# Kernel tuning notes

Hardware: AMD Instinct MI355X
Metric: run time of the kernel (lower is better)

## Reference

```python
import jax, jax.numpy as jnp
import numpy as np

C = 19
IGNORE = 255
UPPER_BOUND = 1.0
SEG_W, EDGE_W, ATT_W = 1.0, 0.3, 0.1
EDGE_THRESH = 0.8


def _img_hist(t):
    # torch.histc(target, bins=C, min=0, max=C): bin i counts values in [i, i+1); 255 falls outside
    tf = t.ravel()
    inb = (tf >= 0) & (tf < C)
    idx = jnp.where(inb, tf, 0)
    return jnp.zeros((C,), jnp.float32).at[idx].add(inb.astype(jnp.float32))


def _seg_loss(segin, target):
    # per-image class-histogram weights (ImageBasedCrossEntropyLoss2d, norm=False)
    N = target.shape[0]
    bins = jax.vmap(_img_hist)(target)                      # [N, C]
    hist_norm = bins / jnp.sum(bins, axis=1, keepdims=True)
    w = (bins != 0).astype(jnp.float32) * UPPER_BOUND * (1.0 - hist_norm) + 1.0  # [N, C]

    logp = jax.nn.log_softmax(segin, axis=1)                # [N, C, H, W]
    tc = jnp.clip(target, 0, C - 1)
    lp = jnp.take_along_axis(logp, tc[:, None, :, :], axis=1)[:, 0]  # [N, H, W]
    valid = (target != IGNORE).astype(jnp.float32)
    pw = jnp.take_along_axis(w, tc.reshape(N, -1), axis=1).reshape(target.shape) * valid
    # NLLLoss(weight, reduction='mean', ignore_index): weighted mean per image, summed over batch
    num = -jnp.sum(pw * lp, axis=(1, 2))
    den = jnp.sum(pw, axis=(1, 2))
    return jnp.sum(num / den)


def _bce2d(x, t):
    # x: logits [N,1,H,W]; t: float target, 1=pos, 0=neg, >1 ignored (weight 0)
    pos = t == 1.0
    neg = t == 0.0
    pos_num = jnp.sum(pos.astype(jnp.float32))
    neg_num = jnp.sum(neg.astype(jnp.float32))
    sum_num = pos_num + neg_num
    w = jnp.where(pos, neg_num / sum_num, 0.0) + jnp.where(neg, pos_num / sum_num, 0.0)
    # stable BCE-with-logits
    bce = jnp.maximum(x, 0.0) - x * t + jnp.log1p(jnp.exp(-jnp.abs(x)))
    return jnp.mean(w * bce)


def setup_inputs() -> dict:
    key = jax.random.key(0)
    k1, k2, k3, k4 = jax.random.split(key, 4)
    N, H, W = 4, 768, 768
    segin = jax.random.normal(k1, (N, C, H, W), dtype=jnp.float32)
    edgein = jax.random.normal(k2, (N, 1, H, W), dtype=jnp.float32)
    segmask = jax.random.randint(k3, (N, H, W), 0, C, dtype=jnp.int32)
    edgemask = jax.random.randint(k4, (N, 1, H, W), 0, 2, dtype=jnp.int32)
    return {"segin": segin, "edgein": edgein, "segmask": segmask, "edgemask": edgemask}


def reference(segin, edgein, segmask, edgemask):
    seg_loss = SEG_W * _seg_loss(segin, segmask)
    edge_loss = EDGE_W * _bce2d(edgein, edgemask.astype(jnp.float32))
    # edge attention: pixels where max-channel edge logit > 0.8 keep their label, else ignore
    edge_max = jnp.max(edgein, axis=1)                      # [N, H, W]
    att_target = jnp.where(edge_max > EDGE_THRESH, segmask, IGNORE)
    att_loss = ATT_W * _seg_loss(segin, att_target)
    return seg_loss + edge_loss + att_loss
```

## Files before the change

kernel.cpp:

```cpp
#include <hip/hip_runtime.h>
#include <math.h>

#define CNUM 19
#define NB 4
#define HW 589824
#define NPIX 2359296

struct Ws {
  unsigned int hist_seg[NB][CNUM];
  unsigned int hist_att[NB][CNUM];
  unsigned int pos_num;
  unsigned int neg_num;
  float w_seg[NB][CNUM];
  float w_att[NB][CNUM];
  double num_seg[NB];
  double den_seg[NB];
  double num_att[NB];
  double den_att[NB];
  double bce_sum;
};

__global__ void k_init(Ws* ws) {
  unsigned int* p = (unsigned int*)ws;
  const int nwords = (int)(sizeof(Ws) / 4);
  for (int i = threadIdx.x; i < nwords; i += blockDim.x) p[i] = 0u;
}

__global__ __launch_bounds__(256) void k_hist(const int* __restrict__ segmask,
                                              const float* __restrict__ edgein,
                                              const int* __restrict__ edgemask,
                                              Ws* ws) {
  __shared__ unsigned int sh[2 * NB * CNUM + 2];
  for (int i = threadIdx.x; i < 2 * NB * CNUM + 2; i += 256) sh[i] = 0u;
  __syncthreads();
  unsigned int* sh_seg = sh;
  unsigned int* sh_att = sh + NB * CNUM;
  unsigned int* sh_pn  = sh + 2 * NB * CNUM;
  const int lane = threadIdx.x & 63;
  const int base0 = blockIdx.x * 256 + threadIdx.x;
  #pragma unroll
  for (int it = 0; it < 9; ++it) {
    int idx = base0 + it * (1024 * 256);
    int n = idx / HW;
    int s = segmask[idx];
    float e = edgein[idx];
    int em = edgemask[idx];
    bool inb = (s >= 0) && (s < CNUM);
    if (inb) atomicAdd(&sh_seg[n * CNUM + s], 1u);
    if (inb && (e > 0.8f)) atomicAdd(&sh_att[n * CNUM + s], 1u);
    unsigned long long bp = __ballot(em == 1);
    unsigned long long bn = __ballot(em == 0);
    if (lane == 0) {
      atomicAdd(&sh_pn[0], (unsigned int)__popcll(bp));
      atomicAdd(&sh_pn[1], (unsigned int)__popcll(bn));
    }
  }
  __syncthreads();
  for (int i = threadIdx.x; i < NB * CNUM; i += 256) {
    if (sh_seg[i]) atomicAdd(&((unsigned int*)ws->hist_seg)[i], sh_seg[i]);
    if (sh_att[i]) atomicAdd(&((unsigned int*)ws->hist_att)[i], sh_att[i]);
  }
  if (threadIdx.x == 0)  atomicAdd(&ws->pos_num, sh_pn[0]);
  if (threadIdx.x == 64) atomicAdd(&ws->neg_num, sh_pn[1]);
}

__global__ void k_weights(Ws* ws) {
  int t = threadIdx.x;
  if (t < 2 * NB * CNUM) {
    int which = t / (NB * CNUM);
    int r = t % (NB * CNUM);
    int n = r / CNUM, c = r % CNUM;
    const unsigned int* h = which ? ws->hist_att[n] : ws->hist_seg[n];
    float total = 0.f;
    #pragma unroll
    for (int i = 0; i < CNUM; ++i) total += (float)h[i];
    float bins = (float)h[c];
    float w = (bins != 0.f ? (1.0f - bins / total) : 0.f) + 1.0f;
    if (which) ws->w_att[n][c] = w;
    else       ws->w_seg[n][c] = w;
  }
}

__global__ __launch_bounds__(256) void k_main(const float* __restrict__ segin,
                                              const float* __restrict__ edgein,
                                              const int* __restrict__ segmask,
                                              const int* __restrict__ edgemask,
                                              Ws* __restrict__ ws) {
  const int n = blockIdx.y;
  const int hw4 = (blockIdx.x * 256 + threadIdx.x) * 4;
  const int idx4 = n * HW + hw4;
  const float* base = segin + (size_t)n * CNUM * HW + hw4;

  float x[CNUM][4];
  #pragma unroll
  for (int c = 0; c < CNUM; ++c) {
    float4 v = *reinterpret_cast<const float4*>(base + (size_t)c * HW);
    x[c][0] = v.x; x[c][1] = v.y; x[c][2] = v.z; x[c][3] = v.w;
  }
  int4   tm = *reinterpret_cast<const int4*>(segmask + idx4);
  float4 ev = *reinterpret_cast<const float4*>(edgein + idx4);
  int4   em = *reinterpret_cast<const int4*>(edgemask + idx4);
  int   tarr[4]  = {tm.x, tm.y, tm.z, tm.w};
  float earr[4]  = {ev.x, ev.y, ev.z, ev.w};
  int   emarr[4] = {em.x, em.y, em.z, em.w};

  const unsigned int pn = ws->pos_num, nn = ws->neg_num;
  const float inv_sum = 1.0f / (float)(pn + nn);
  const float wpos = (float)nn * inv_sum;
  const float wneg = (float)pn * inv_sum;

  float acc_num_s = 0.f, acc_den_s = 0.f, acc_num_a = 0.f, acc_den_a = 0.f, acc_bce = 0.f;
  #pragma unroll
  for (int p = 0; p < 4; ++p) {
    int t = tarr[p];
    int tc = min(max(t, 0), CNUM - 1);
    float m = x[0][p];
    #pragma unroll
    for (int c = 1; c < CNUM; ++c) m = fmaxf(m, x[c][p]);
    float s = 0.f;
    #pragma unroll
    for (int c = 0; c < CNUM; ++c) s += __expf(x[c][p] - m);
    float lse = m + __logf(s);
    float xt = x[0][p];
    #pragma unroll
    for (int c = 1; c < CNUM; ++c) xt = (tc == c) ? x[c][p] : xt;
    float lp = xt - lse;

    bool validt = (t != 255);
    float pw_s = validt ? ws->w_seg[n][tc] : 0.f;
    acc_num_s -= pw_s * lp;
    acc_den_s += pw_s;

    float e = earr[p];
    bool valida = validt && (e > 0.8f);
    float pw_a = valida ? ws->w_att[n][tc] : 0.f;
    acc_num_a -= pw_a * lp;
    acc_den_a += pw_a;

    int emv = emarr[p];
    float tf = (float)emv;
    float wb = (emv == 1) ? wpos : ((emv == 0) ? wneg : 0.f);
    float bce = fmaxf(e, 0.f) - e * tf + log1pf(__expf(-fabsf(e)));
    acc_bce += wb * bce;
  }

  #pragma unroll
  for (int off = 32; off > 0; off >>= 1) {
    acc_num_s += __shfl_down(acc_num_s, off);
    acc_den_s += __shfl_down(acc_den_s, off);
    acc_num_a += __shfl_down(acc_num_a, off);
    acc_den_a += __shfl_down(acc_den_a, off);
    acc_bce   += __shfl_down(acc_bce, off);
  }
  __shared__ float red[4][5];
  const int wave = threadIdx.x >> 6;
  const int lane = threadIdx.x & 63;
  if (lane == 0) {
    red[wave][0] = acc_num_s; red[wave][1] = acc_den_s;
    red[wave][2] = acc_num_a; red[wave][3] = acc_den_a;
    red[wave][4] = acc_bce;
  }
  __syncthreads();
  if (threadIdx.x == 0) {
    float r0 = 0.f, r1 = 0.f, r2 = 0.f, r3 = 0.f, r4 = 0.f;
    #pragma unroll
    for (int wv = 0; wv < 4; ++wv) {
      r0 += red[wv][0]; r1 += red[wv][1]; r2 += red[wv][2];
      r3 += red[wv][3]; r4 += red[wv][4];
    }
    atomicAdd(&ws->num_seg[n], (double)r0);
    atomicAdd(&ws->den_seg[n], (double)r1);
    atomicAdd(&ws->num_att[n], (double)r2);
    atomicAdd(&ws->den_att[n], (double)r3);
    atomicAdd(&ws->bce_sum,    (double)r4);
  }
}

__global__ void k_final(const Ws* __restrict__ ws, float* __restrict__ out) {
  if (threadIdx.x == 0 && blockIdx.x == 0) {
    double segl = 0.0, attl = 0.0;
    for (int i = 0; i < NB; ++i) {
      segl += ws->num_seg[i] / ws->den_seg[i];
      attl += ws->num_att[i] / ws->den_att[i];
    }
    double edgel = ws->bce_sum / (double)NPIX;
    out[0] = (float)(1.0 * segl + 0.3 * edgel + 0.1 * attl);
  }
}

extern "C" void kernel_launch(void* const* d_in, const int* in_sizes, int n_in,
                              void* d_out, int out_size, void* d_ws, size_t ws_size,
                              hipStream_t stream) {
  const float* segin   = (const float*)d_in[0];
  const float* edgein  = (const float*)d_in[1];
  const int*   segmask = (const int*)d_in[2];
  const int*   edgemask= (const int*)d_in[3];
  Ws* ws = (Ws*)d_ws;
  float* out = (float*)d_out;

  hipLaunchKernelGGL(k_init,    dim3(1),            dim3(256), 0, stream, ws);
  hipLaunchKernelGGL(k_hist,    dim3(1024),         dim3(256), 0, stream, segmask, edgein, edgemask, ws);
  hipLaunchKernelGGL(k_weights, dim3(1),            dim3(256), 0, stream, ws);
  hipLaunchKernelGGL(k_main,    dim3(HW / 1024, NB), dim3(256), 0, stream, segin, edgein, segmask, edgemask, ws);
  hipLaunchKernelGGL(k_final,   dim3(1),            dim3(1),   0, stream, ws, out);
}
```

Baseline: 364.7 us.

## Stream softmax without max pass and rework histogram with wave ballots

After: 355.8 us. 1.02x faster.

```diff
diff --git a/kernel.cpp b/kernel.cpp
--- a/kernel.cpp
+++ b/kernel.cpp
@@ -29,39 +29,58 @@
 __global__ __launch_bounds__(256) void k_hist(const int* __restrict__ segmask,
                                               const float* __restrict__ edgein,
                                               const int* __restrict__ edgemask,
-                                              Ws* ws) {
-  __shared__ unsigned int sh[2 * NB * CNUM + 2];
-  for (int i = threadIdx.x; i < 2 * NB * CNUM + 2; i += 256) sh[i] = 0u;
+                                              Ws* __restrict__ ws) {
+  const int n  = blockIdx.y;
+  const int bx = blockIdx.x;
+  const int tid = threadIdx.x;
+  const int base = n * HW + bx * 4096 + tid * 4;
+
+  unsigned int cs[CNUM], ca[CNUM];
+  #pragma unroll
+  for (int c = 0; c < CNUM; ++c) { cs[c] = 0u; ca[c] = 0u; }
+  unsigned int cp = 0u, cn = 0u;
+
+  #pragma unroll
+  for (int it = 0; it < 4; ++it) {
+    const int idx = base + it * 1024;
+    int4   sv = *reinterpret_cast<const int4*>(segmask + idx);
+    float4 e  = *reinterpret_cast<const float4*>(edgein + idx);
+    int4   mv = *reinterpret_cast<const int4*>(edgemask + idx);
+    int   sa[4] = {sv.x, sv.y, sv.z, sv.w};
+    float ea[4] = {e.x, e.y, e.z, e.w};
+    int   ma[4] = {mv.x, mv.y, mv.z, mv.w};
+    #pragma unroll
+    for (int p = 0; p < 4; ++p) {
+      const int s = sa[p];
+      const bool inb = ((unsigned)s) < (unsigned)CNUM;
+      const bool att = inb && (ea[p] > 0.8f);
+      #pragma unroll
+      for (int c = 0; c < CNUM; ++c) {
+        cs[c] += (unsigned)__popcll(__ballot(inb && (s == c)));
+        ca[c] += (unsigned)__popcll(__ballot(att && (s == c)));
+      }
+      cp += (unsigned)__popcll(__ballot(ma[p] == 1));
+      cn += (unsigned)__popcll(__ballot(ma[p] == 0));
+    }
+  }
+
+  __shared__ unsigned int red[4][2 * CNUM + 2];
+  const int wave = tid >> 6;
+  const int lane = tid & 63;
+  if (lane == 0) {
+    #pragma unroll
+    for (int c = 0; c < CNUM; ++c) { red[wave][c] = cs[c]; red[wave][CNUM + c] = ca[c]; }
+    red[wave][2 * CNUM] = cp;
+    red[wave][2 * CNUM + 1] = cn;
+  }
   __syncthreads();
-  unsigned int* sh_seg = sh;
-  unsigned int* sh_att = sh + NB * CNUM;
-  unsigned int* sh_pn  = sh + 2 * NB * CNUM;
-  const int lane = threadIdx.x & 63;
-  const int base0 = blockIdx.x * 256 + threadIdx.x;
-  #pragma unroll
-  for (int it = 0; it < 9; ++it) {
-    int idx = base0 + it * (1024 * 256);
-    int n = idx / HW;
-    int s = segmask[idx];
-    float e = edgein[idx];
-    int em = edgemask[idx];
-    bool inb = (s >= 0) && (s < CNUM);
-    if (inb) atomicAdd(&sh_seg[n * CNUM + s], 1u);
-    if (inb && (e > 0.8f)) atomicAdd(&sh_att[n * CNUM + s], 1u);
-    unsigned long long bp = __ballot(em == 1);
-    unsigned long long bn = __ballot(em == 0);
-    if (lane == 0) {
-      atomicAdd(&sh_pn[0], (unsigned int)__popcll(bp));
-      atomicAdd(&sh_pn[1], (unsigned int)__popcll(bn));
-    }
-  }
-  __syncthreads();
-  for (int i = threadIdx.x; i < NB * CNUM; i += 256) {
-    if (sh_seg[i]) atomicAdd(&((unsigned int*)ws->hist_seg)[i], sh_seg[i]);
-    if (sh_att[i]) atomicAdd(&((unsigned int*)ws->hist_att)[i], sh_att[i]);
-  }
-  if (threadIdx.x == 0)  atomicAdd(&ws->pos_num, sh_pn[0]);
-  if (threadIdx.x == 64) atomicAdd(&ws->neg_num, sh_pn[1]);
+  if (tid < 2 * CNUM + 2) {
+    unsigned int v = red[0][tid] + red[1][tid] + red[2][tid] + red[3][tid];
+    if (tid < CNUM)               atomicAdd(&ws->hist_seg[n][tid], v);
+    else if (tid < 2 * CNUM)      atomicAdd(&ws->hist_att[n][tid - CNUM], v);
+    else if (tid == 2 * CNUM)     atomicAdd(&ws->pos_num, v);
+    else                          atomicAdd(&ws->neg_num, v);
+  }
 }
 
 __global__ void k_weights(Ws* ws) {
@@ -85,18 +104,19 @@
                                               const float* __restrict__ edgein,
                                               const int* __restrict__ segmask,
                                               const int* __restrict__ edgemask,
-                                              Ws* __restrict__ ws) {
+                                              const Ws* __restrict__ ws,
+                                              Ws* __restrict__ wsw) {
   const int n = blockIdx.y;
-  const int hw4 = (blockIdx.x * 256 + threadIdx.x) * 4;
+  const int tid = threadIdx.x;
+  const int hw4 = (blockIdx.x * 256 + tid) * 4;
   const int idx4 = n * HW + hw4;
   const float* base = segin + (size_t)n * CNUM * HW + hw4;
 
-  float x[CNUM][4];
-  #pragma unroll
-  for (int c = 0; c < CNUM; ++c) {
-    float4 v = *reinterpret_cast<const float4*>(base + (size_t)c * HW);
-    x[c][0] = v.x; x[c][1] = v.y; x[c][2] = v.z; x[c][3] = v.w;
-  }
+  __shared__ float lws[CNUM], lwa[CNUM];
+  if (tid < CNUM) lws[tid] = ws->w_seg[n][tid];
+  else if (tid >= 64 && tid < 64 + CNUM) lwa[tid - 64] = ws->w_att[n][tid - 64];
+  __syncthreads();
+
   int4   tm = *reinterpret_cast<const int4*>(segmask + idx4);
   float4 ev = *reinterpret_cast<const float4*>(edgein + idx4);
   int4   em = *reinterpret_cast<const int4*>(edgemask + idx4);
@@ -104,6 +124,23 @@
   float earr[4]  = {ev.x, ev.y, ev.z, ev.w};
   int   emarr[4] = {em.x, em.y, em.z, em.w};
 
+  int tc[4];
+  #pragma unroll
+  for (int p = 0; p < 4; ++p) tc[p] = min(max(tarr[p], 0), CNUM - 1);
+
+  float s[4]  = {0.f, 0.f, 0.f, 0.f};
+  float xt[4] = {0.f, 0.f, 0.f, 0.f};
+  #pragma unroll
+  for (int c = 0; c < CNUM; ++c) {
+    float4 v = *reinterpret_cast<const float4*>(base + (size_t)c * HW);
+    float va[4] = {v.x, v.y, v.z, v.w};
+    #pragma unroll
+    for (int p = 0; p < 4; ++p) {
+      s[p] += __expf(va[p]);
+      xt[p] = (tc[p] == c) ? va[p] : xt[p];
+    }
+  }
+
   const unsigned int pn = ws->pos_num, nn = ws->neg_num;
   const float inv_sum = 1.0f / (float)(pn + nn);
   const float wpos = (float)nn * inv_sum;
@@ -112,28 +149,15 @@
   float acc_num_s = 0.f, acc_den_s = 0.f, acc_num_a = 0.f, acc_den_a = 0.f, acc_bce = 0.f;
   #pragma unroll
   for (int p = 0; p < 4; ++p) {
-    int t = tarr[p];
-    int tc = min(max(t, 0), CNUM - 1);
-    float m = x[0][p];
-    #pragma unroll
-    for (int c = 1; c < CNUM; ++c) m = fmaxf(m, x[c][p]);
-    float s = 0.f;
-    #pragma unroll
-    for (int c = 0; c < CNUM; ++c) s += __expf(x[c][p] - m);
-    float lse = m + __logf(s);
-    float xt = x[0][p];
-    #pragma unroll
-    for (int c = 1; c < CNUM; ++c) xt = (tc == c) ? x[c][p] : xt;
-    float lp = xt - lse;
-
-    bool validt = (t != 255);
-    float pw_s = validt ? ws->w_seg[n][tc] : 0.f;
+    float lp = xt[p] - __logf(s[p]);
+    bool validt = (tarr[p] != 255);
+    float pw_s = validt ? lws[tc[p]] : 0.f;
     acc_num_s -= pw_s * lp;
     acc_den_s += pw_s;
 
     float e = earr[p];
     bool valida = validt && (e > 0.8f);
-    float pw_a = valida ? ws->w_att[n][tc] : 0.f;
+    float pw_a = valida ? lwa[tc[p]] : 0.f;
     acc_num_a -= pw_a * lp;
     acc_den_a += pw_a;
 
@@ -153,26 +177,26 @@
     acc_bce   += __shfl_down(acc_bce, off);
   }
   __shared__ float red[4][5];
-  const int wave = threadIdx.x >> 6;
-  const int lane = threadIdx.x & 63;
+  const int wave = tid >> 6;
+  const int lane = tid & 63;
   if (lane == 0) {
     red[wave][0] = acc_num_s; red[wave][1] = acc_den_s;
     red[wave][2] = acc_num_a; red[wave][3] = acc_den_a;
     red[wave][4] = acc_bce;
   }
   __syncthreads();
-  if (threadIdx.x == 0) {
+  if (tid == 0) {
     float r0 = 0.f, r1 = 0.f, r2 = 0.f, r3 = 0.f, r4 = 0.f;
     #pragma unroll
     for (int wv = 0; wv < 4; ++wv) {
       r0 += red[wv][0]; r1 += red[wv][1]; r2 += red[wv][2];
       r3 += red[wv][3]; r4 += red[wv][4];
     }
-    atomicAdd(&ws->num_seg[n], (double)r0);
-    atomicAdd(&ws->den_seg[n], (double)r1);
-    atomicAdd(&ws->num_att[n], (double)r2);
-    atomicAdd(&ws->den_att[n], (double)r3);
-    atomicAdd(&ws->bce_sum,    (double)r4);
+    atomicAdd(&wsw->num_seg[n], (double)r0);
+    atomicAdd(&wsw->den_seg[n], (double)r1);
+    atomicAdd(&wsw->num_att[n], (double)r2);
+    atomicAdd(&wsw->den_att[n], (double)r3);
+    atomicAdd(&wsw->bce_sum,    (double)r4);
   }
 }
 
@@ -198,9 +222,9 @@
   Ws* ws = (Ws*)d_ws;
   float* out = (float*)d_out;
 
-  hipLaunchKernelGGL(k_init,    dim3(1),            dim3(256), 0, stream, ws);
-  hipLaunchKernelGGL(k_hist,    dim3(1024),         dim3(256), 0, stream, segmask, edgein, edgemask, ws);
-  hipLaunchKernelGGL(k_weights, dim3(1),            dim3(256), 0, stream, ws);
-  hipLaunchKernelGGL(k_main,    dim3(HW / 1024, NB), dim3(256), 0, stream, segin, edgein, segmask, edgemask, ws);
-  hipLaunchKernelGGL(k_final,   dim3(1),            dim3(1),   0, stream, ws, out);
-}
+  hipLaunchKernelGGL(k_init,    dim3(1),              dim3(256), 0, stream, ws);
+  hipLaunchKernelGGL(k_hist,    dim3(HW / 4096, NB),  dim3(256), 0, stream, segmask, edgein, edgemask, ws);
+  hipLaunchKernelGGL(k_weights, dim3(1),              dim3(256), 0, stream, ws);
+  hipLaunchKernelGGL(k_main,    dim3(HW / 1024, NB),  dim3(256), 0, stream, segin, edgein, segmask, edgemask, ws, ws);
+  hipLaunchKernelGGL(k_final,   dim3(1),              dim3(1),   0, stream, ws, out);
+}
```
